# Performance work log

Hardware: AMD Instinct MI355X
Metric: run time of the kernel (lower is better)

Reference implementation:

```python
import jax, jax.numpy as jnp
import numpy as np

B, S, DIN, DOUT, A, T, H = 8, 1024, 1024, 1024, 4, 4, 8  # arity A, T cell types, hidden H


def setup_inputs() -> dict:
    key = jax.random.key(0)
    ks = jax.random.split(key, 6)
    x = jax.random.normal(ks[0], (B, S, DIN), jnp.float32)
    sc = 1.0 / np.sqrt(DIN).astype(np.float32)
    weight = jax.random.uniform(ks[1], (A * DOUT, DIN), jnp.float32, -sc, sc)
    bias = jax.random.uniform(ks[2], (A * DOUT,), jnp.float32, -sc, sc)
    # stacked per-cell-type MLP params: arity -> H -> 1 (tanh)
    cw1 = jax.random.normal(ks[3], (T, A, H), jnp.float32) / np.sqrt(A).astype(np.float32)
    cb1 = jnp.zeros((T, H), jnp.float32)
    cw2 = jax.random.normal(ks[4], (T, H), jnp.float32) / np.sqrt(H).astype(np.float32)
    cb2 = jnp.zeros((T,), jnp.float32)
    return {"x": x, "weight": weight, "bias": bias,
            "cw1": cw1, "cb1": cb1, "cw2": cw2, "cb2": cb2}


def reference(x, weight, bias, cw1, cb1, cw2, cb2):
    T_, A_, H_ = cw1.shape
    Dout = weight.shape[0] // A_
    G = Dout // T_  # neurons per cell type (cell_indices = contiguous blocks via np.repeat)
    # all_inputs = F.linear(input, weight, bias): (B, S, A*Dout)
    z = jnp.einsum('bsd,od->bso', x, weight) + bias
    # slice per-neuron arity chunks -> (B, S, T, G, A)
    z = z.reshape(z.shape[0], z.shape[1], T_, G, A_)
    # per-cell-type MLP applied to every neuron of that type (replaces Python loop)
    h = jnp.tanh(jnp.einsum('bstga,tah->bstgh', z, cw1) + cb1[:, None, :])
    o = jnp.einsum('bstgh,th->bstg', h, cw2) + cb2[:, None]
    # concat over neurons -> (B, S, Dout)
    return o.reshape(o.shape[0], o.shape[1], Dout)
```

## Files before the change

kernel.cpp:

```cpp
#include <hip/hip_runtime.h>


typedef __bf16 bf16x8 __attribute__((ext_vector_type(8)));
typedef float f32x4 __attribute__((ext_vector_type(4)));
typedef float f32x16 __attribute__((ext_vector_type(16)));

#define BM 256
#define BN 128
#define BK 64
#define KDIM 1024
#define A_ELEMS (BM * BK)
#define ZSTRIDE 132
#define XN8 (8192 * 1024 / 8)
#define WN8 (4096 * 1024 / 8)

__global__ __launch_bounds__(256) void cvt_bf16_kernel(
    const float* __restrict__ x, const float* __restrict__ w,
    __bf16* __restrict__ xb, __bf16* __restrict__ wb) {
    int i = blockIdx.x * 256 + threadIdx.x;
    const float* src;
    __bf16* dst;
    int j;
    if (i < XN8) { src = x; dst = xb; j = i; }
    else         { src = w; dst = wb; j = i - XN8; }
    const f32x4* p = (const f32x4*)src + 2 * (size_t)j;
    f32x4 a = p[0], b = p[1];
    bf16x8 o;
    o[0] = (__bf16)a[0]; o[1] = (__bf16)a[1]; o[2] = (__bf16)a[2]; o[3] = (__bf16)a[3];
    o[4] = (__bf16)b[0]; o[5] = (__bf16)b[1]; o[6] = (__bf16)b[2]; o[7] = (__bf16)b[3];
    ((bf16x8*)dst)[j] = o;
}

union __align__(16) SmemU {
    __bf16 stg[A_ELEMS + BN * BK];
    float  z[64 * ZSTRIDE];
};

__global__ __launch_bounds__(256, 2) void fused_gemm_mlp_kernel(
    const __bf16* __restrict__ Ag,
    const __bf16* __restrict__ Bg,
    const float* __restrict__ bias,
    const float* __restrict__ cw1,
    const float* __restrict__ cb1,
    const float* __restrict__ cw2,
    const float* __restrict__ cb2,
    float* __restrict__ out)
{
    __shared__ SmemU u;

    const int tid  = threadIdx.x;
    const int wave = tid >> 6;
    const int lane = tid & 63;
    const int wm = wave >> 1;
    const int wn = wave & 1;
    const int bn0 = blockIdx.x * BN;
    const int bm0 = blockIdx.y * BM;

    f32x16 acc[4][2] = {};

    const int srow  = lane >> 3;
    const int scol8 = (((lane & 7) ^ srow) * 8);

    const int lr5 = lane & 31;
    const int lk2 = lane >> 5;
    const int lx  = lane & 7;
    int a_base[4], b_base[4];
#pragma unroll
    for (int kh = 0; kh < 4; ++kh) {
        const int cx = ((kh * 2 + lk2) ^ lx) * 16;
        a_base[kh] = (wm * 128 + lr5) * (BK * 2) + cx;
        b_base[kh] = A_ELEMS * 2 + (wn * 64 + lr5) * (BK * 2) + cx;
    }
    const char* sb = (const char*)u.stg;

    for (int k0 = 0; k0 < KDIM; k0 += BK) {
#pragma unroll
        for (int c = 0; c < 8; ++c) {
            const int chunk = wave + c * 4;
            const __bf16* ga = Ag + (size_t)(bm0 + chunk * 8 + srow) * KDIM + k0 + scol8;
            __builtin_amdgcn_global_load_lds(
                (__attribute__((address_space(1))) void*)ga,
                (__attribute__((address_space(3))) void*)&u.stg[chunk * 8 * BK],
                16, 0, 0);
        }
#pragma unroll
        for (int c = 0; c < 4; ++c) {
            const int chunk = wave + c * 4;
            const __bf16* gb = Bg + (size_t)(bn0 + chunk * 8 + srow) * KDIM + k0 + scol8;
            __builtin_amdgcn_global_load_lds(
                (__attribute__((address_space(1))) void*)gb,
                (__attribute__((address_space(3))) void*)&u.stg[A_ELEMS + chunk * 8 * BK],
                16, 0, 0);
        }
        __syncthreads();

#pragma unroll
        for (int kh = 0; kh < 4; ++kh) {
            bf16x8 af[4], bfr[2];
#pragma unroll
            for (int mi = 0; mi < 4; ++mi)
                af[mi] = *(const bf16x8*)(sb + a_base[kh] + mi * 4096);
#pragma unroll
            for (int ni = 0; ni < 2; ++ni)
                bfr[ni] = *(const bf16x8*)(sb + b_base[kh] + ni * 4096);
#pragma unroll
            for (int mi = 0; mi < 4; ++mi)
#pragma unroll
                for (int ni = 0; ni < 2; ++ni)
                    acc[mi][ni] = __builtin_amdgcn_mfma_f32_32x32x16_bf16(
                        af[mi], bfr[ni], acc[mi][ni], 0, 0, 0);
        }
        __syncthreads();
    }

    const int t = bn0 >> 10;
    float w1[32], b1[8], w2[8];
#pragma unroll
    for (int i = 0; i < 32; ++i) w1[i] = cw1[t * 32 + i];
#pragma unroll
    for (int i = 0; i < 8; ++i) { b1[i] = cb1[t * 8 + i]; w2[i] = cw2[t * 8 + i]; }
    const float b2 = cb2[t];

    float bcol[2];
#pragma unroll
    for (int ni = 0; ni < 2; ++ni)
        bcol[ni] = bias[bn0 + wn * 64 + ni * 32 + lr5];

    const float L2E2 = 2.885390081777927f;

#pragma unroll
    for (int h = 0; h < 4; ++h) {
        if (wm == (h >> 1)) {
            const int mi0 = (h & 1) * 2;
#pragma unroll
            for (int dmi = 0; dmi < 2; ++dmi) {
                const int mi = mi0 + dmi;
#pragma unroll
                for (int ni = 0; ni < 2; ++ni) {
                    const int n = wn * 64 + ni * 32 + lr5;
#pragma unroll
                    for (int g = 0; g < 4; ++g) {
                        const int rb = dmi * 32 + g * 8 + lk2 * 4;
                        u.z[(rb + 0) * ZSTRIDE + n] = acc[mi][ni][g * 4 + 0] + bcol[ni];
                        u.z[(rb + 1) * ZSTRIDE + n] = acc[mi][ni][g * 4 + 1] + bcol[ni];
                        u.z[(rb + 2) * ZSTRIDE + n] = acc[mi][ni][g * 4 + 2] + bcol[ni];
                        u.z[(rb + 3) * ZSTRIDE + n] = acc[mi][ni][g * 4 + 3] + bcol[ni];
                    }
                }
            }
        }
        __syncthreads();

#pragma unroll
        for (int it = 0; it < 8; ++it) {
            const int i = tid + it * 256;
            const int q = i & 31;
            const int r = i >> 5;
            f32x4 z = *(const f32x4*)&u.z[r * ZSTRIDE + 4 * q];
            float o = 0.f;
#pragma unroll
            for (int hh = 0; hh < 8; ++hh) {
                float pre = z[0] * w1[0 * 8 + hh] + z[1] * w1[1 * 8 + hh]
                          + z[2] * w1[2 * 8 + hh] + z[3] * w1[3 * 8 + hh] + b1[hh];
                float e = __builtin_amdgcn_exp2f(pre * L2E2);
                float th = 1.0f - 2.0f * __builtin_amdgcn_rcpf(e + 1.0f);
                o += th * w2[hh];
            }
            o += b2;
            out[(size_t)(bm0 + h * 64 + r) * 1024 + (bn0 >> 2) + q] = o;
        }
        __syncthreads();
    }
}

extern "C" void kernel_launch(void* const* d_in, const int* in_sizes, int n_in,
                              void* d_out, int out_size, void* d_ws, size_t ws_size,
                              hipStream_t stream) {
    const float* x    = (const float*)d_in[0];
    const float* w    = (const float*)d_in[1];
    const float* bias = (const float*)d_in[2];
    const float* cw1  = (const float*)d_in[3];
    const float* cb1  = (const float*)d_in[4];
    const float* cw2  = (const float*)d_in[5];
    const float* cb2  = (const float*)d_in[6];
    float* out = (float*)d_out;

    __bf16* xb = (__bf16*)d_ws;
    __bf16* wb = xb + (size_t)8192 * 1024;

    cvt_bf16_kernel<<<(XN8 + WN8) / 256, 256, 0, stream>>>(x, w, xb, wb);

    dim3 grid(4096 / BN, 8192 / BM);
    fused_gemm_mlp_kernel<<<grid, 256, 0, stream>>>(xb, wb, bias, cw1, cb1, cw2, cb2, out);
}
```

Baseline: 188.1 us.

## Double-buffer LDS staging, widen tile to 256x256 with 8 waves, fold tanh constants

The GEMM tile grows to 256x256, computed by 512 threads (8 waves in a 2x4 layout). Two LDS stage buffers let the next K-slice's global-to-LDS loads be issued before the current slice's MFMAs, leaving one barrier per iteration instead of two. The tanh/MLP epilogue pre-scales w1 and b1 by 2*log2(e) and folds the constant terms into the output initializer, which removes a multiply and an add per hidden unit. LDS use rises to 128KB per block, which likely allows only one block per CU despite the launch bound of 2, and the grid halves to 16x32 blocks.

```diff
diff --git a/kernel.cpp b/kernel.cpp
--- a/kernel.cpp
+++ b/kernel.cpp
@@ -6,11 +6,13 @@
 typedef float f32x16 __attribute__((ext_vector_type(16)));
 
 #define BM 256
-#define BN 128
+#define BN 256
 #define BK 64
 #define KDIM 1024
-#define A_ELEMS (BM * BK)
-#define ZSTRIDE 132
+#define NITER (KDIM / BK)
+#define BUF_ELEMS 32768
+#define BUF_BYTES 65536
+#define ZS 260
 #define XN8 (8192 * 1024 / 8)
 #define WN8 (4096 * 1024 / 8)
 
@@ -32,11 +34,11 @@
 }
 
 union __align__(16) SmemU {
-    __bf16 stg[A_ELEMS + BN * BK];
-    float  z[64 * ZSTRIDE];
+    __bf16 stg[2 * BUF_ELEMS];
+    float  z[64 * ZS];
 };
 
-__global__ __launch_bounds__(256, 2) void fused_gemm_mlp_kernel(
+__global__ __launch_bounds__(512, 2) void fused_gemm_mlp_kernel(
     const __bf16* __restrict__ Ag,
     const __bf16* __restrict__ Bg,
     const float* __restrict__ bias,
@@ -51,15 +53,15 @@
     const int tid  = threadIdx.x;
     const int wave = tid >> 6;
     const int lane = tid & 63;
-    const int wm = wave >> 1;
-    const int wn = wave & 1;
+    const int wm = wave >> 2;
+    const int wn = wave & 3;
     const int bn0 = blockIdx.x * BN;
     const int bm0 = blockIdx.y * BM;
 
     f32x16 acc[4][2] = {};
 
     const int srow  = lane >> 3;
-    const int scol8 = (((lane & 7) ^ srow) * 8);
+    const int scol8 = ((lane & 7) ^ srow) * 8;
 
     const int lr5 = lane & 31;
     const int lk2 = lane >> 5;
@@ -68,41 +70,45 @@
 #pragma unroll
     for (int kh = 0; kh < 4; ++kh) {
         const int cx = ((kh * 2 + lk2) ^ lx) * 16;
-        a_base[kh] = (wm * 128 + lr5) * (BK * 2) + cx;
-        b_base[kh] = A_ELEMS * 2 + (wn * 64 + lr5) * (BK * 2) + cx;
+        a_base[kh] = (wm * 128 + lr5) * 128 + cx;
+        b_base[kh] = 32768 + (wn * 64 + lr5) * 128 + cx;
     }
     const char* sb = (const char*)u.stg;
 
-    for (int k0 = 0; k0 < KDIM; k0 += BK) {
-#pragma unroll
-        for (int c = 0; c < 8; ++c) {
-            const int chunk = wave + c * 4;
-            const __bf16* ga = Ag + (size_t)(bm0 + chunk * 8 + srow) * KDIM + k0 + scol8;
+    auto stage = [&](int it, int buf) {
+        __bf16* dstA = u.stg + buf * BUF_ELEMS;
+        __bf16* dstB = dstA + 16384;
+        const int kof = it * BK;
+#pragma unroll
+        for (int c = 0; c < 4; ++c) {
+            const int chunk = wave + c * 8;
+            const __bf16* ga = Ag + (size_t)(bm0 + chunk * 8 + srow) * KDIM + kof + scol8;
             __builtin_amdgcn_global_load_lds(
                 (__attribute__((address_space(1))) void*)ga,
-                (__attribute__((address_space(3))) void*)&u.stg[chunk * 8 * BK],
+                (__attribute__((address_space(3))) void*)&dstA[chunk * 512],
                 16, 0, 0);
-        }
-#pragma unroll
-        for (int c = 0; c < 4; ++c) {
-            const int chunk = wave + c * 4;
-            const __bf16* gb = Bg + (size_t)(bn0 + chunk * 8 + srow) * KDIM + k0 + scol8;
+            const __bf16* gb = Bg + (size_t)(bn0 + chunk * 8 + srow) * KDIM + kof + scol8;
             __builtin_amdgcn_global_load_lds(
                 (__attribute__((address_space(1))) void*)gb,
-                (__attribute__((address_space(3))) void*)&u.stg[A_ELEMS + chunk * 8 * BK],
+                (__attribute__((address_space(3))) void*)&dstB[chunk * 512],
                 16, 0, 0);
         }
+    };
+
+    stage(0, 0);
+    for (int it = 0; it < NITER; ++it) {
         __syncthreads();
-
+        if (it + 1 < NITER) stage(it + 1, (it + 1) & 1);
+        const int bufo = (it & 1) * BUF_BYTES;
 #pragma unroll
         for (int kh = 0; kh < 4; ++kh) {
             bf16x8 af[4], bfr[2];
 #pragma unroll
             for (int mi = 0; mi < 4; ++mi)
-                af[mi] = *(const bf16x8*)(sb + a_base[kh] + mi * 4096);
+                af[mi] = *(const bf16x8*)(sb + bufo + a_base[kh] + mi * 4096);
 #pragma unroll
             for (int ni = 0; ni < 2; ++ni)
-                bfr[ni] = *(const bf16x8*)(sb + b_base[kh] + ni * 4096);
+                bfr[ni] = *(const bf16x8*)(sb + bufo + b_base[kh] + ni * 4096);
 #pragma unroll
             for (int mi = 0; mi < 4; ++mi)
 #pragma unroll
@@ -110,41 +116,43 @@
                     acc[mi][ni] = __builtin_amdgcn_mfma_f32_32x32x16_bf16(
                         af[mi], bfr[ni], acc[mi][ni], 0, 0, 0);
         }
-        __syncthreads();
-    }
+    }
+    __syncthreads();
 
     const int t = bn0 >> 10;
-    float w1[32], b1[8], w2[8];
-#pragma unroll
-    for (int i = 0; i < 32; ++i) w1[i] = cw1[t * 32 + i];
-#pragma unroll
-    for (int i = 0; i < 8; ++i) { b1[i] = cb1[t * 8 + i]; w2[i] = cw2[t * 8 + i]; }
-    const float b2 = cb2[t];
+    const float L2E2 = 2.885390081777927f;
+    float w1s[32], b1s[8], w2m[8];
+#pragma unroll
+    for (int i = 0; i < 32; ++i) w1s[i] = cw1[t * 32 + i] * L2E2;
+    float oinit = cb2[t];
+#pragma unroll
+    for (int i = 0; i < 8; ++i) {
+        b1s[i] = cb1[t * 8 + i] * L2E2;
+        w2m[i] = -2.0f * cw2[t * 8 + i];
+        oinit += cw2[t * 8 + i];
+    }
 
     float bcol[2];
 #pragma unroll
     for (int ni = 0; ni < 2; ++ni)
         bcol[ni] = bias[bn0 + wn * 64 + ni * 32 + lr5];
 
-    const float L2E2 = 2.885390081777927f;
-
 #pragma unroll
     for (int h = 0; h < 4; ++h) {
         if (wm == (h >> 1)) {
-            const int mi0 = (h & 1) * 2;
 #pragma unroll
             for (int dmi = 0; dmi < 2; ++dmi) {
-                const int mi = mi0 + dmi;
+                const int mi = (h & 1) * 2 + dmi;
 #pragma unroll
                 for (int ni = 0; ni < 2; ++ni) {
                     const int n = wn * 64 + ni * 32 + lr5;
 #pragma unroll
                     for (int g = 0; g < 4; ++g) {
                         const int rb = dmi * 32 + g * 8 + lk2 * 4;
-                        u.z[(rb + 0) * ZSTRIDE + n] = acc[mi][ni][g * 4 + 0] + bcol[ni];
-                        u.z[(rb + 1) * ZSTRIDE + n] = acc[mi][ni][g * 4 + 1] + bcol[ni];
-                        u.z[(rb + 2) * ZSTRIDE + n] = acc[mi][ni][g * 4 + 2] + bcol[ni];
-                        u.z[(rb + 3) * ZSTRIDE + n] = acc[mi][ni][g * 4 + 3] + bcol[ni];
+                        u.z[(rb + 0) * ZS + n] = acc[mi][ni][g * 4 + 0] + bcol[ni];
+                        u.z[(rb + 1) * ZS + n] = acc[mi][ni][g * 4 + 1] + bcol[ni];
+                        u.z[(rb + 2) * ZS + n] = acc[mi][ni][g * 4 + 2] + bcol[ni];
+                        u.z[(rb + 3) * ZS + n] = acc[mi][ni][g * 4 + 3] + bcol[ni];
                     }
                 }
             }
@@ -152,21 +160,19 @@
         __syncthreads();
 
 #pragma unroll
-        for (int it = 0; it < 8; ++it) {
-            const int i = tid + it * 256;
-            const int q = i & 31;
-            const int r = i >> 5;
-            f32x4 z = *(const f32x4*)&u.z[r * ZSTRIDE + 4 * q];
-            float o = 0.f;
+        for (int it2 = 0; it2 < 8; ++it2) {
+            const int i = tid + it2 * 512;
+            const int q = i & 63;
+            const int r = i >> 6;
+            f32x4 z = *(const f32x4*)&u.z[r * ZS + 4 * q];
+            float o = oinit;
 #pragma unroll
             for (int hh = 0; hh < 8; ++hh) {
-                float pre = z[0] * w1[0 * 8 + hh] + z[1] * w1[1 * 8 + hh]
-                          + z[2] * w1[2 * 8 + hh] + z[3] * w1[3 * 8 + hh] + b1[hh];
-                float e = __builtin_amdgcn_exp2f(pre * L2E2);
-                float th = 1.0f - 2.0f * __builtin_amdgcn_rcpf(e + 1.0f);
-                o += th * w2[hh];
+                float pre = z[0] * w1s[0 * 8 + hh] + z[1] * w1s[1 * 8 + hh]
+                          + z[2] * w1s[2 * 8 + hh] + z[3] * w1s[3 * 8 + hh] + b1s[hh];
+                float e = __builtin_amdgcn_exp2f(pre);
+                o += w2m[hh] * __builtin_amdgcn_rcpf(e + 1.0f);
             }
-            o += b2;
             out[(size_t)(bm0 + h * 64 + r) * 1024 + (bn0 >> 2) + q] = o;
         }
         __syncthreads();
@@ -191,5 +197,5 @@
     cvt_bf16_kernel<<<(XN8 + WN8) / 256, 256, 0, stream>>>(x, w, xb, wb);
 
     dim3 grid(4096 / BN, 8192 / BM);
-    fused_gemm_mlp_kernel<<<grid, 256, 0, stream>>>(xb, wb, bias, cw1, cb1, cw2, cb2, out);
+    fused_gemm_mlp_kernel<<<grid, 512, 0, stream>>>(xb, wb, bias, cw1, cb1, cw2, cb2, out);
 }
```

Result: no change. 190.5 us (+1.3%).
